# Optimization experiments

Hardware: AMD Instinct MI355X
Metric: run time of the kernel (lower is better)

## Reference

```python
import jax, jax.numpy as jnp
import numpy as np

D_MODEL = 1024
N_HEADS = 16
D_HEAD = D_MODEL // N_HEADS


def setup_inputs() -> dict:
    key = jax.random.key(0)
    ks = jax.random.split(key, 11)
    B, L = 2, 2048
    s = 1.0 / np.sqrt(D_MODEL)
    return {
        "query": jax.random.normal(ks[0], (B, L, D_MODEL), jnp.float32),
        "key": jax.random.normal(ks[1], (B, L, D_MODEL), jnp.float32),
        "value": jax.random.normal(ks[2], (B, L, D_MODEL), jnp.float32),
        "Wq": jax.random.normal(ks[3], (D_MODEL, D_MODEL), jnp.float32) * s,
        "bq": jnp.zeros((D_MODEL,), jnp.float32),
        "Wk": jax.random.normal(ks[4], (D_MODEL, D_MODEL), jnp.float32) * s,
        "bk": jnp.zeros((D_MODEL,), jnp.float32),
        "Wv": jax.random.normal(ks[5], (D_MODEL, D_MODEL), jnp.float32) * s,
        "bv": jnp.zeros((D_MODEL,), jnp.float32),
        "Wo": jax.random.normal(ks[6], (D_MODEL, D_MODEL), jnp.float32) * s,
        "bo": jnp.zeros((D_MODEL,), jnp.float32),
    }


def reference(query, key, value, Wq, bq, Wk, bk, Wv, bv, Wo, bo):
    B, Lq, _ = query.shape
    Lk = key.shape[1]
    scale = D_HEAD ** -0.5
    # projections; weights stored as [in, out] (torch Linear applies x @ W.T; here W is already transposed)
    q = (query @ Wq + bq).reshape(B, Lq, N_HEADS, D_HEAD).transpose(0, 2, 1, 3)  # [B,H,Lq,dh]
    k = (key @ Wk + bk).reshape(B, Lk, N_HEADS, D_HEAD).transpose(0, 2, 1, 3)
    v = (value @ Wv + bv).reshape(B, Lk, N_HEADS, D_HEAD).transpose(0, 2, 1, 3)
    scores = jnp.einsum('bhqd,bhkd->bhqk', q, k) * scale  # [B,H,Lq,Lk]
    # causal mask (is_causal=True)
    causal = jnp.triu(jnp.ones((Lq, Lk), dtype=bool), k=1)
    scores = jnp.where(causal, -jnp.inf, scores)
    attn = jax.nn.softmax(scores, axis=-1)
    out = jnp.einsum('bhqk,bhkd->bhqd', attn, v)  # [B,H,Lq,dh]
    out = out.transpose(0, 2, 1, 3).reshape(B, Lq, D_MODEL)
    return out @ Wo + bo
```

## Files before the change

kernel.cpp:

```cpp
#include <hip/hip_runtime.h>
#include <hip/hip_bf16.h>

typedef __bf16 bf16x8 __attribute__((ext_vector_type(8)));
typedef __bf16 bf16x4 __attribute__((ext_vector_type(4)));
typedef float floatx4 __attribute__((ext_vector_type(4)));

#define MFMA16(a, b, c) __builtin_amdgcn_mfma_f32_16x16x32_bf16(a, b, c, 0, 0, 0)
#define AS1 __attribute__((address_space(1)))
#define AS3 __attribute__((address_space(3)))

constexpr int D = 1024;
constexpr int L = 2048;
constexpr int BB = 2;
constexpr int DH = 64;
constexpr float NEG_BIG = -1e30f;
constexpr float SCALE_LOG2E = 0.125f * 1.4426950408889634f;

__device__ __forceinline__ void gld16(const __bf16* g, __bf16* l) {
  __builtin_amdgcn_global_load_lds((AS1 void*)g, (AS3 void*)l, 16, 0, 0);
}

__global__ __launch_bounds__(256) void prep(const float* __restrict__ xq, const float* __restrict__ xk,
                                            const float* __restrict__ xv,
                                            const float* __restrict__ w0, const float* __restrict__ w1,
                                            const float* __restrict__ w2, const float* __restrict__ w3,
                                            __bf16* __restrict__ xc, __bf16* __restrict__ wt) {
  const int z = blockIdx.z;
  const int t = threadIdx.x;
  if (z < 3) {
    const float* src = z == 0 ? xq : z == 1 ? xk : xv;
    __bf16* dst = xc + (size_t)z * BB * L * D;
    const int N = BB * L * D;
    const int stride = gridDim.x * 256 * 4;
    for (int i = (blockIdx.x * 256 + t) * 4; i < N; i += stride) {
      float4 f = *(const float4*)&src[i];
      bf16x4 b = {(__bf16)f.x, (__bf16)f.y, (__bf16)f.z, (__bf16)f.w};
      *(bf16x4*)&dst[i] = b;
    }
  } else {
    __shared__ __bf16 tile[32][33];
    const int mat = z - 3;
    const float* src = mat == 0 ? w0 : mat == 1 ? w1 : mat == 2 ? w2 : w3;
    __bf16* dst = wt + (size_t)mat * D * D;
    const int bx = (blockIdx.x & 31) * 32, by = (blockIdx.x >> 5) * 32;
    const int tx = t & 31, ty = t >> 5;
#pragma unroll
    for (int i = 0; i < 32; i += 8)
      tile[ty + i][tx] = (__bf16)src[(size_t)(by + ty + i) * D + bx + tx];
    __syncthreads();
#pragma unroll
    for (int i = 0; i < 32; i += 8)
      dst[(size_t)(bx + ty + i) * D + by + tx] = tile[tx][ty + i];
  }
}

__device__ __forceinline__ void stage32(const __bf16* __restrict__ A, const __bf16* __restrict__ Bt,
                                        __bf16* sA, __bf16* sB, int m0, int n0, int kb,
                                        int r, int sc, int dst) {
  gld16(&A[(size_t)(m0 + r) * 1024 + kb + sc],       &sA[dst]);
  gld16(&A[(size_t)(m0 + 64 + r) * 1024 + kb + sc],  &sA[2048 + dst]);
  gld16(&Bt[(size_t)(n0 + r) * 1024 + kb + sc],      &sB[dst]);
  gld16(&Bt[(size_t)(n0 + 64 + r) * 1024 + kb + sc], &sB[2048 + dst]);
}

__device__ __forceinline__ void gemm_core(const __bf16* __restrict__ A, const __bf16* __restrict__ Bt,
                                          __bf16* sm, int m0, int n0, int wm, int wn,
                                          int l15, int quad, int t, floatx4 (&acc)[4][4]) {
  const int r = t >> 2;
  const int sc = ((t & 3) ^ ((r >> 1) & 3)) * 8;
  const int dst = t * 8;
  const int sw2 = (l15 >> 1) & 3;

  stage32(A, Bt, sm, sm + 8192, m0, n0, 0, r, sc, dst);

  int cur = 0;
  for (int kb = 0; kb < 1024; kb += 32) {
    if (kb + 32 < 1024) {
      stage32(A, Bt, sm + (cur ^ 1) * 4096, sm + 8192 + (cur ^ 1) * 4096, m0, n0, kb + 32, r, sc, dst);
      asm volatile("s_waitcnt vmcnt(4)" ::: "memory");
    } else {
      asm volatile("s_waitcnt vmcnt(0)" ::: "memory");
    }
    __builtin_amdgcn_s_barrier();

    const __bf16* sAc = sm + cur * 4096;
    const __bf16* sBc = sm + 8192 + cur * 4096;
    bf16x8 af[4], bf_[4];
#pragma unroll
    for (int i = 0; i < 4; i++) {
      const int row = wm * 64 + i * 16 + l15;
      af[i] = *(const bf16x8*)&sAc[(row * 4 + (quad ^ sw2)) * 8];
    }
#pragma unroll
    for (int j = 0; j < 4; j++) {
      const int row = wn * 64 + j * 16 + l15;
      bf_[j] = *(const bf16x8*)&sBc[(row * 4 + (quad ^ sw2)) * 8];
    }
    asm volatile("s_waitcnt lgkmcnt(0)" ::: "memory");
    __builtin_amdgcn_sched_barrier(0);
    __builtin_amdgcn_s_barrier();

#pragma unroll
    for (int i = 0; i < 4; i++)
#pragma unroll
      for (int j = 0; j < 4; j++)
        acc[i][j] = MFMA16(af[i], bf_[j], acc[i][j]);

    cur ^= 1;
  }
}

__global__ __launch_bounds__(256, 3) void gemm_proj(const __bf16* __restrict__ xc, const __bf16* __restrict__ wt,
                                                    const float* __restrict__ bq, const float* __restrict__ bk,
                                                    const float* __restrict__ bv, __bf16* __restrict__ qkv) {
  __shared__ __align__(16) __bf16 smem[17408];

  const int flat = (blockIdx.z * 32 + blockIdx.y) * 8 + blockIdx.x;
  const int s = (flat & 7) * 96 + (flat >> 3);
  const int z = s >> 8;
  const int rem = s & 255;
  const int by = rem >> 3, bx = rem & 7;

  const __bf16* A = xc + (size_t)z * BB * L * D;
  const __bf16* Bt = wt + (size_t)z * D * D;
  const float* bias = z == 0 ? bq : z == 1 ? bk : bv;
  __bf16* dst = qkv + (size_t)z * BB * L * D;

  const int t = threadIdx.x;
  const int lane = t & 63;
  const int w = t >> 6;
  const int wm = w >> 1, wn = w & 1;
  const int l15 = lane & 15, quad = lane >> 4;
  const int m0 = by * 128, n0 = bx * 128;

  floatx4 acc[4][4];
#pragma unroll
  for (int i = 0; i < 4; i++)
#pragma unroll
    for (int j = 0; j < 4; j++) acc[i][j] = (floatx4){0.f, 0.f, 0.f, 0.f};

  gemm_core(A, Bt, smem, m0, n0, wm, wn, l15, quad, t, acc);

  float bvv[4];
#pragma unroll
  for (int j = 0; j < 4; j++) bvv[j] = bias[n0 + wn * 64 + j * 16 + l15];

  constexpr int TP = 136;
  __bf16* T = smem;
  if (z < 2) {
#pragma unroll
    for (int i = 0; i < 4; i++) {
      const int mrowb = wm * 64 + i * 16 + quad * 4;
#pragma unroll
      for (int j = 0; j < 4; j++) {
        const int ccol = wn * 64 + j * 16 + l15;
#pragma unroll
        for (int rr = 0; rr < 4; rr++) {
          float val = acc[i][j][rr] + bvv[j];
          if (z == 0) val *= SCALE_LOG2E;
          T[(mrowb + rr) * TP + ccol] = (__bf16)val;
        }
      }
    }
  } else {
#pragma unroll
    for (int i = 0; i < 4; i++) {
      const int mrowp = wm * 64 + (i >> 1) * 32 + quad * 8 + (i & 1) * 4;
#pragma unroll
      for (int j = 0; j < 4; j++) {
        const int ccol = wn * 64 + j * 16 + l15;
        bf16x4 v4;
#pragma unroll
        for (int rr = 0; rr < 4; rr++) v4[rr] = (__bf16)(acc[i][j][rr] + bvv[j]);
        *(bf16x4*)&T[ccol * TP + mrowp] = v4;
      }
    }
  }
  __syncthreads();

  const int b = m0 >> 11;
  const int l0 = m0 & 2047;
  if (z < 2) {
#pragma unroll
    for (int sH = 0; sH < 8; sH++) {
      const int c = sH * 256 + t;
      const int mrow = c >> 4, k16 = c & 15;
      const int h = (n0 >> 6) + (k16 >> 3);
      const int d0 = (k16 & 7) * 8;
      bf16x8 v = *(const bf16x8*)&T[mrow * TP + k16 * 8];
      *(bf16x8*)&dst[((size_t)(b * 16 + h) * 2048 + l0 + mrow) * 64 + d0] = v;
    }
  } else {
    const int R0 = (b * 16 + (n0 >> 6)) * 64;
#pragma unroll
    for (int sH = 0; sH < 8; sH++) {
      const int c = sH * 256 + t;
      const int ccol = c >> 4, k16 = c & 15;
      bf16x8 v = *(const bf16x8*)&T[ccol * TP + k16 * 8];
      *(bf16x8*)&dst[(size_t)(R0 + ccol) * 2048 + l0 + k16 * 8] = v;
    }
  }
}

__global__ __launch_bounds__(256, 3) void gemm_o(const __bf16* __restrict__ ctx, const __bf16* __restrict__ wto,
                                                 const float* __restrict__ bo, float* __restrict__ out) {
  __shared__ __align__(16) __bf16 smem[16384];

  const int flat = blockIdx.y * 8 + blockIdx.x;
  const int s = (flat & 7) * 32 + (flat >> 3);
  const int by = s >> 3, bx = s & 7;

  const int t = threadIdx.x;
  const int lane = t & 63;
  const int w = t >> 6;
  const int wm = w >> 1, wn = w & 1;
  const int l15 = lane & 15, quad = lane >> 4;
  const int m0 = by * 128, n0 = bx * 128;

  floatx4 acc[4][4];
#pragma unroll
  for (int i = 0; i < 4; i++)
#pragma unroll
    for (int j = 0; j < 4; j++) acc[i][j] = (floatx4){0.f, 0.f, 0.f, 0.f};

  gemm_core(ctx, wto, smem, m0, n0, wm, wn, l15, quad, t, acc);

  float bvv[4];
#pragma unroll
  for (int j = 0; j < 4; j++) bvv[j] = bo[n0 + wn * 64 + j * 16 + l15];

#pragma unroll
  for (int i = 0; i < 4; i++) {
    const int rowb = m0 + wm * 64 + i * 16 + quad * 4;
#pragma unroll
    for (int j = 0; j < 4; j++) {
      const int col = n0 + wn * 64 + j * 16 + l15;
#pragma unroll
      for (int rr = 0; rr < 4; rr++)
        out[(size_t)(rowb + rr) * 1024 + col] = acc[i][j][rr] + bvv[j];
    }
  }
}

__global__ __launch_bounds__(256, 2) void flash_attn(const __bf16* __restrict__ q, const __bf16* __restrict__ k,
                                                     const __bf16* __restrict__ vT, __bf16* __restrict__ ctx) {
  __shared__ __align__(16) __bf16 kbuf[2][2][4096];
  __shared__ __align__(16) __bf16 vbuf[2][2][4096];

  const int t = threadIdx.x;
  const int lane = t & 63;
  const int w = t >> 6;
  const int l15 = lane & 15, quad = lane >> 4;
  const int bh = blockIdx.y;
  const int p = (blockIdx.x + blockIdx.y) & 15;
  const int qtA = 31 - p;
  const int qtB = p;

  const __bf16* qb = q + (size_t)bh * L * DH;
  const __bf16* kb_ = k + (size_t)bh * L * DH;
  const __bf16* vb = vT + (size_t)bh * DH * L;

  const int c0 = t, c1 = 256 + t;
  const int kr0 = c0 >> 3, kd0 = ((c0 & 7) ^ (kr0 & 7)) * 8;
  const int kr1 = c1 >> 3, kd1 = ((c1 & 7) ^ (kr1 & 7)) * 8;

  const int qrA = qtA * 64 + w * 16 + l15;
  const int qrB = qtB * 64 + w * 16 + l15;
  const bf16x8 aqA0 = *(const bf16x8*)&qb[(size_t)qrA * 64 + quad * 8];
  const bf16x8 aqA1 = *(const bf16x8*)&qb[(size_t)qrA * 64 + 32 + quad * 8];
  const bf16x8 aqB0 = *(const bf16x8*)&qb[(size_t)qrB * 64 + quad * 8];
  const bf16x8 aqB1 = *(const bf16x8*)&qb[(size_t)qrB * 64 + 32 + quad * 8];

  floatx4 oA[4], oB[4];
#pragma unroll
  for (int nt = 0; nt < 4; nt++) {
    oA[nt] = (floatx4){0.f, 0.f, 0.f, 0.f};
    oB[nt] = (floatx4){0.f, 0.f, 0.f, 0.f};
  }
  float psA = 0.f, psB = 0.f;

  auto STAGE = [&](int buf, int half, int ktile) {
    const int kt = ktile * 64;
    gld16(&kb_[(size_t)(kt + kr0) * 64 + kd0], &kbuf[buf][half][c0 * 8]);
    gld16(&kb_[(size_t)(kt + kr1) * 64 + kd1], &kbuf[buf][half][c1 * 8]);
    gld16(&vb[(size_t)kr0 * L + kt + kd0],     &vbuf[buf][half][c0 * 8]);
    gld16(&vb[(size_t)kr1 * L + kt + kd1],     &vbuf[buf][half][c1 * 8]);
  };

  auto COMPUTE = [&](int buf, int half, int ktile) {
    const int kt = ktile * 64;
    const bool diagA = (ktile == qtA);
    const bool doB   = (ktile <= qtB);
    const bool diagB = (ktile == qtB);
    const __bf16* kbh = kbuf[buf][half];
    const __bf16* vbh = vbuf[buf][half];

#pragma unroll
    for (int sp = 0; sp < 2; ++sp) {
      bf16x8 kf0[2], kf1[2];
#pragma unroll
      for (int u = 0; u < 2; ++u) {
        const int kr = (2 * sp + u) * 16 + l15;
        kf0[u] = *(const bf16x8*)&kbh[(kr * 8 + (quad ^ (kr & 7))) * 8];
        kf1[u] = *(const bf16x8*)&kbh[(kr * 8 + ((quad + 4) ^ (kr & 7))) * 8];
      }

      bf16x8 paA;
#pragma unroll
      for (int u = 0; u < 2; ++u) {
        floatx4 zz = (floatx4){0.f, 0.f, 0.f, 0.f};
        zz = MFMA16(kf0[u], aqA0, zz);
        zz = MFMA16(kf1[u], aqA1, zz);
        if (diagA) {
          const int kgb = kt + (2 * sp + u) * 16 + quad * 4;
#pragma unroll
          for (int rr = 0; rr < 4; rr++)
            if (kgb + rr > qrA) zz[rr] = NEG_BIG;
        }
#pragma unroll
        for (int rr = 0; rr < 4; rr++) {
          const float pv = __builtin_amdgcn_exp2f(zz[rr]);
          psA += pv;
          paA[u * 4 + rr] = (__bf16)pv;
        }
      }

      bf16x8 paB;
      if (doB) {
#pragma unroll
        for (int u = 0; u < 2; ++u) {
          floatx4 zz = (floatx4){0.f, 0.f, 0.f, 0.f};
          zz = MFMA16(kf0[u], aqB0, zz);
          zz = MFMA16(kf1[u], aqB1, zz);
          if (diagB) {
            const int kgb = kt + (2 * sp + u) * 16 + quad * 4;
#pragma unroll
            for (int rr = 0; rr < 4; rr++)
              if (kgb + rr > qrB) zz[rr] = NEG_BIG;
          }
#pragma unroll
          for (int rr = 0; rr < 4; rr++) {
            const float pv = __builtin_amdgcn_exp2f(zz[rr]);
            psB += pv;
            paB[u * 4 + rr] = (__bf16)pv;
          }
        }
      }

#pragma unroll
      for (int nt = 0; nt < 4; nt++) {
        const int d = nt * 16 + l15;
        const int x = (sp * 4 + quad) ^ (d & 7);
        const bf16x8 vv = *(const bf16x8*)&vbh[(d * 8 + x) * 8];
        oA[nt] = MFMA16(paA, vv, oA[nt]);
        if (doB) oB[nt] = MFMA16(paB, vv, oB[nt]);
      }
    }
  };

  const int ntiles = qtA + 1;
  STAGE(0, 0, 0);
  STAGE(0, 1, 1);

  int it2 = 0;
#pragma unroll 1
  for (int base = 0; base < ntiles; base += 2, ++it2) {
    const int cur = it2 & 1;
    const int remn = ntiles - base - 2;

    if (remn >= 2) {
      STAGE(cur ^ 1, 0, base + 2);
      STAGE(cur ^ 1, 1, base + 3);
      asm volatile("s_waitcnt vmcnt(8)" ::: "memory");
    } else if (remn == 1) {
      STAGE(cur ^ 1, 0, base + 2);
      asm volatile("s_waitcnt vmcnt(4)" ::: "memory");
    } else {
      asm volatile("s_waitcnt vmcnt(0)" ::: "memory");
    }
    __builtin_amdgcn_s_barrier();

    COMPUTE(cur, 0, base);
    if (base + 1 < ntiles) COMPUTE(cur, 1, base + 1);

    asm volatile("s_waitcnt lgkmcnt(0)" ::: "memory");
    __builtin_amdgcn_sched_barrier(0);
    __builtin_amdgcn_s_barrier();
  }

  const int b = bh >> 4, h = bh & 15;

  psA += __shfl_xor(psA, 16);
  psA += __shfl_xor(psA, 32);
  const float invA = 1.f / psA;
#pragma unroll
  for (int rr = 0; rr < 4; rr++) {
    const float inv = __shfl(invA, (lane & 48) + quad * 4 + rr);
    const int row = qtA * 64 + w * 16 + quad * 4 + rr;
#pragma unroll
    for (int nt = 0; nt < 4; nt++) {
      const int col = h * 64 + nt * 16 + l15;
      ctx[((size_t)b * L + row) * 1024 + col] = (__bf16)(oA[nt][rr] * inv);
    }
  }

  psB += __shfl_xor(psB, 16);
  psB += __shfl_xor(psB, 32);
  const float invB = 1.f / psB;
#pragma unroll
  for (int rr = 0; rr < 4; rr++) {
    const float inv = __shfl(invB, (lane & 48) + quad * 4 + rr);
    const int row = qtB * 64 + w * 16 + quad * 4 + rr;
#pragma unroll
    for (int nt = 0; nt < 4; nt++) {
      const int col = h * 64 + nt * 16 + l15;
      ctx[((size_t)b * L + row) * 1024 + col] = (__bf16)(oB[nt][rr] * inv);
    }
  }
}

extern "C" void kernel_launch(void* const* d_in, const int* in_sizes, int n_in,
                              void* d_out, int out_size, void* d_ws, size_t ws_size,
                              hipStream_t stream) {
  const float* x_q = (const float*)d_in[0];
  const float* x_k = (const float*)d_in[1];
  const float* x_v = (const float*)d_in[2];
  const float* Wq  = (const float*)d_in[3];
  const float* bq  = (const float*)d_in[4];
  const float* Wk  = (const float*)d_in[5];
  const float* bk  = (const float*)d_in[6];
  const float* Wv  = (const float*)d_in[7];
  const float* bv  = (const float*)d_in[8];
  const float* Wo  = (const float*)d_in[9];
  const float* bo  = (const float*)d_in[10];

  char* ws = (char*)d_ws;
  __bf16* xc  = (__bf16*)ws;
  __bf16* wt  = (__bf16*)(ws + ((size_t)24 << 20));
  __bf16* qkv = (__bf16*)(ws + ((size_t)32 << 20));
  __bf16* ctx = (__bf16*)ws;
  __bf16* qp  = qkv;
  __bf16* kp  = qkv + (size_t)BB * L * D;
  __bf16* vtp = qkv + (size_t)2 * BB * L * D;

  prep<<<dim3(1024, 1, 7), 256, 0, stream>>>(x_q, x_k, x_v, Wq, Wk, Wv, Wo, xc, wt);
  gemm_proj<<<dim3(8, 32, 3), 256, 0, stream>>>(xc, wt, bq, bk, bv, qkv);
  flash_attn<<<dim3(16, 32), 256, 0, stream>>>(qp, kp, vtp, ctx);
  gemm_o<<<dim3(8, 32), 256, 0, stream>>>(ctx, wt + (size_t)3 * D * D, bo, (float*)d_out);
}
```

Before: 203.7 us.

## Fuse fp32-to-bf16 activation conversion into projection GEMM A-tile loads

Measured after the change: 217.0 us. 1.07x slower.

```diff
diff --git a/kernel.cpp b/kernel.cpp
--- a/kernel.cpp
+++ b/kernel.cpp
@@ -20,38 +20,30 @@
   __builtin_amdgcn_global_load_lds((AS1 void*)g, (AS3 void*)l, 16, 0, 0);
 }
 
-__global__ __launch_bounds__(256) void prep(const float* __restrict__ xq, const float* __restrict__ xk,
-                                            const float* __restrict__ xv,
-                                            const float* __restrict__ w0, const float* __restrict__ w1,
+__device__ __forceinline__ bf16x8 cvt8(const float4& x, const float4& y) {
+  bf16x8 o;
+  o[0] = (__bf16)x.x; o[1] = (__bf16)x.y; o[2] = (__bf16)x.z; o[3] = (__bf16)x.w;
+  o[4] = (__bf16)y.x; o[5] = (__bf16)y.y; o[6] = (__bf16)y.z; o[7] = (__bf16)y.w;
+  return o;
+}
+
+__global__ __launch_bounds__(256) void prep(const float* __restrict__ w0, const float* __restrict__ w1,
                                             const float* __restrict__ w2, const float* __restrict__ w3,
-                                            __bf16* __restrict__ xc, __bf16* __restrict__ wt) {
-  const int z = blockIdx.z;
+                                            __bf16* __restrict__ wt) {
+  __shared__ __bf16 tile[32][33];
   const int t = threadIdx.x;
-  if (z < 3) {
-    const float* src = z == 0 ? xq : z == 1 ? xk : xv;
-    __bf16* dst = xc + (size_t)z * BB * L * D;
-    const int N = BB * L * D;
-    const int stride = gridDim.x * 256 * 4;
-    for (int i = (blockIdx.x * 256 + t) * 4; i < N; i += stride) {
-      float4 f = *(const float4*)&src[i];
-      bf16x4 b = {(__bf16)f.x, (__bf16)f.y, (__bf16)f.z, (__bf16)f.w};
-      *(bf16x4*)&dst[i] = b;
-    }
-  } else {
-    __shared__ __bf16 tile[32][33];
-    const int mat = z - 3;
-    const float* src = mat == 0 ? w0 : mat == 1 ? w1 : mat == 2 ? w2 : w3;
-    __bf16* dst = wt + (size_t)mat * D * D;
-    const int bx = (blockIdx.x & 31) * 32, by = (blockIdx.x >> 5) * 32;
-    const int tx = t & 31, ty = t >> 5;
-#pragma unroll
-    for (int i = 0; i < 32; i += 8)
-      tile[ty + i][tx] = (__bf16)src[(size_t)(by + ty + i) * D + bx + tx];
-    __syncthreads();
-#pragma unroll
-    for (int i = 0; i < 32; i += 8)
-      dst[(size_t)(bx + ty + i) * D + by + tx] = tile[tx][ty + i];
-  }
+  const int mat = blockIdx.z;
+  const float* src = mat == 0 ? w0 : mat == 1 ? w1 : mat == 2 ? w2 : w3;
+  __bf16* dst = wt + (size_t)mat * D * D;
+  const int bx = (blockIdx.x & 31) * 32, by = (blockIdx.x >> 5) * 32;
+  const int tx = t & 31, ty = t >> 5;
+#pragma unroll
+  for (int i = 0; i < 32; i += 8)
+    tile[ty + i][tx] = (__bf16)src[(size_t)(by + ty + i) * D + bx + tx];
+  __syncthreads();
+#pragma unroll
+  for (int i = 0; i < 32; i += 8)
+    dst[(size_t)(bx + ty + i) * D + by + tx] = tile[tx][ty + i];
 }
 
 __device__ __forceinline__ void stage32(const __bf16* __restrict__ A, const __bf16* __restrict__ Bt,
@@ -110,7 +102,84 @@
   }
 }
 
-__global__ __launch_bounds__(256, 3) void gemm_proj(const __bf16* __restrict__ xc, const __bf16* __restrict__ wt,
+__device__ __forceinline__ void gemm_core_xf32(const float* __restrict__ Ax, const __bf16* __restrict__ Bt,
+                                               __bf16* sm, int m0, int n0, int wm, int wn,
+                                               int l15, int quad, int t, floatx4 (&acc)[4][4]) {
+  const int r = t >> 2;
+  const int sc = ((t & 3) ^ ((r >> 1) & 3)) * 8;
+  const int dst = t * 8;
+  const int sw2 = (l15 >> 1) & 3;
+
+  const float* a0p = &Ax[(size_t)(m0 + r) * 1024 + sc];
+  const float* a1p = &Ax[(size_t)(m0 + 64 + r) * 1024 + sc];
+
+  float4 a00 = *(const float4*)&a0p[0], a01 = *(const float4*)&a0p[4];
+  float4 a10 = *(const float4*)&a1p[0], a11 = *(const float4*)&a1p[4];
+  __builtin_amdgcn_sched_barrier(0);
+  gld16(&Bt[(size_t)(n0 + r) * 1024 + sc],      &sm[8192 + dst]);
+  gld16(&Bt[(size_t)(n0 + 64 + r) * 1024 + sc], &sm[8192 + 2048 + dst]);
+  __builtin_amdgcn_sched_barrier(0);
+  asm volatile("s_waitcnt vmcnt(2)" ::: "memory");
+  *(bf16x8*)&sm[dst]        = cvt8(a00, a01);
+  *(bf16x8*)&sm[2048 + dst] = cvt8(a10, a11);
+  asm volatile("s_waitcnt lgkmcnt(0)" ::: "memory");
+
+  int cur = 0;
+#pragma unroll 1
+  for (int kb = 0; kb < 1024; kb += 32) {
+    const bool has_next = (kb + 32 < 1024);
+    if (has_next) {
+      a00 = *(const float4*)&a0p[kb + 32];
+      a01 = *(const float4*)&a0p[kb + 36];
+      a10 = *(const float4*)&a1p[kb + 32];
+      a11 = *(const float4*)&a1p[kb + 36];
+      __builtin_amdgcn_sched_barrier(0);
+      __bf16* sB1 = sm + 8192 + (cur ^ 1) * 4096;
+      gld16(&Bt[(size_t)(n0 + r) * 1024 + kb + 32 + sc],      &sB1[dst]);
+      gld16(&Bt[(size_t)(n0 + 64 + r) * 1024 + kb + 32 + sc], &sB1[2048 + dst]);
+      __builtin_amdgcn_sched_barrier(0);
+      asm volatile("s_waitcnt vmcnt(6)" ::: "memory");
+    } else {
+      asm volatile("s_waitcnt vmcnt(0)" ::: "memory");
+    }
+    __builtin_amdgcn_s_barrier();
+
+    const __bf16* sAc = sm + cur * 4096;
+    const __bf16* sBc = sm + 8192 + cur * 4096;
+    bf16x8 af[4], bf_[4];
+#pragma unroll
+    for (int i = 0; i < 4; i++) {
+      const int row = wm * 64 + i * 16 + l15;
+      af[i] = *(const bf16x8*)&sAc[(row * 4 + (quad ^ sw2)) * 8];
+    }
+#pragma unroll
+    for (int j = 0; j < 4; j++) {
+      const int row = wn * 64 + j * 16 + l15;
+      bf_[j] = *(const bf16x8*)&sBc[(row * 4 + (quad ^ sw2)) * 8];
+    }
+
+#pragma unroll
+    for (int i = 0; i < 4; i++)
+#pragma unroll
+      for (int j = 0; j < 4; j++)
+        acc[i][j] = MFMA16(af[i], bf_[j], acc[i][j]);
+
+    if (has_next) {
+      asm volatile("s_waitcnt vmcnt(2)" ::: "memory");
+      __bf16* sA1 = sm + (cur ^ 1) * 4096;
+      *(bf16x8*)&sA1[dst]        = cvt8(a00, a01);
+      *(bf16x8*)&sA1[2048 + dst] = cvt8(a10, a11);
+    }
+    asm volatile("s_waitcnt lgkmcnt(0)" ::: "memory");
+    __builtin_amdgcn_sched_barrier(0);
+    __builtin_amdgcn_s_barrier();
+
+    cur ^= 1;
+  }
+}
+
+__global__ __launch_bounds__(256, 3) void gemm_proj(const float* __restrict__ xq, const float* __restrict__ xk,
+                                                    const float* __restrict__ xv, const __bf16* __restrict__ wt,
                                                     const float* __restrict__ bq, const float* __restrict__ bk,
                                                     const float* __restrict__ bv, __bf16* __restrict__ qkv) {
   __shared__ __align__(16) __bf16 smem[17408];
@@ -121,7 +190,7 @@
   const int rem = s & 255;
   const int by = rem >> 3, bx = rem & 7;
 
-  const __bf16* A = xc + (size_t)z * BB * L * D;
+  const float* Ax = z == 0 ? xq : z == 1 ? xk : xv;
   const __bf16* Bt = wt + (size_t)z * D * D;
   const float* bias = z == 0 ? bq : z == 1 ? bk : bv;
   __bf16* dst = qkv + (size_t)z * BB * L * D;
@@ -139,7 +208,7 @@
 #pragma unroll
     for (int j = 0; j < 4; j++) acc[i][j] = (floatx4){0.f, 0.f, 0.f, 0.f};
 
-  gemm_core(A, Bt, smem, m0, n0, wm, wn, l15, quad, t, acc);
+  gemm_core_xf32(Ax, Bt, smem, m0, n0, wm, wn, l15, quad, t, acc);
 
   float bvv[4];
 #pragma unroll
@@ -435,7 +504,6 @@
   const float* bo  = (const float*)d_in[10];
 
   char* ws = (char*)d_ws;
-  __bf16* xc  = (__bf16*)ws;
   __bf16* wt  = (__bf16*)(ws + ((size_t)24 << 20));
   __bf16* qkv = (__bf16*)(ws + ((size_t)32 << 20));
   __bf16* ctx = (__bf16*)ws;
@@ -443,8 +511,8 @@
   __bf16* kp  = qkv + (size_t)BB * L * D;
   __bf16* vtp = qkv + (size_t)2 * BB * L * D;
 
-  prep<<<dim3(1024, 1, 7), 256, 0, stream>>>(x_q, x_k, x_v, Wq, Wk, Wv, Wo, xc, wt);
-  gemm_proj<<<dim3(8, 32, 3), 256, 0, stream>>>(xc, wt, bq, bk, bv, qkv);
+  prep<<<dim3(1024, 1, 4), 256, 0, stream>>>(Wq, Wk, Wv, Wo, wt);
+  gemm_proj<<<dim3(8, 32, 3), 256, 0, stream>>>(x_q, x_k, x_v, wt, bq, bk, bv, qkv);
   flash_attn<<<dim3(16, 32), 256, 0, stream>>>(qp, kp, vtp, ctx);
   gemm_o<<<dim3(8, 32), 256, 0, stream>>>(ctx, wt + (size_t)3 * D * D, bo, (float*)d_out);
 }
```
